# Kernel optimization log

Hardware: AMD Instinct MI355X
Metric: run time of the kernel (lower is better)

## Reference

```python
import jax, jax.numpy as jnp
import numpy as np

B, T, D, L = 8, 8192, 256, 3
DISTS = (1, 5, 15, 30)


def _layernorm(x, g, b, eps=1e-5):
    m = x.mean(-1, keepdims=True)
    v = ((x - m) ** 2).mean(-1, keepdims=True)
    return (x - m) * jax.lax.rsqrt(v + eps) * g + b


def _temporal_edges():
    src, dst = [], []
    for d in DISTS:
        a = np.arange(T - d)
        src += [a, a + d]
        dst += [a + d, a]
    ei = np.stack([np.concatenate(src), np.concatenate(dst)])  # [2, E]
    off = (np.arange(B) * T).repeat(ei.shape[1])
    return np.tile(ei, (1, B)) + off[None, :]  # [2, B*E]


def setup_inputs() -> dict:
    key = jax.random.key(0)
    ks = jax.random.split(key, 6)
    s = 1.0 / np.sqrt(D)
    s4 = 1.0 / np.sqrt(4 * D)
    return dict(
        x=jax.random.normal(ks[0], (B, T, D), jnp.float32),
        adjacency=jnp.zeros((T, T), jnp.float32),  # shape-check only
        edge_index=jnp.asarray(_temporal_edges(), jnp.int32),
        conv_w=jax.random.normal(ks[1], (L, D, D), jnp.float32) * s,
        conv_b=jnp.zeros((L, D), jnp.float32),
        norm_g=jnp.ones((L, D), jnp.float32),
        norm_b=jnp.zeros((L, D), jnp.float32),
        normff_g=jnp.ones((D,), jnp.float32),
        normff_b=jnp.zeros((D,), jnp.float32),
        w1=jax.random.normal(ks[2], (D, 4 * D), jnp.float32) * s,
        b1=jnp.zeros((4 * D,), jnp.float32),
        w2=jax.random.normal(ks[3], (4 * D, D), jnp.float32) * s4,
        b2=jnp.zeros((D,), jnp.float32),
    )


def reference(x, adjacency, edge_index, conv_w, conv_b, norm_g, norm_b,
              normff_g, normff_b, w1, b1, w2, b2):
    b, t, d = x.shape
    n = b * t
    xf = x.reshape(n, d)
    src, dst = edge_index[0], edge_index[1]
    # GCN symmetric degree normalization (no self loops), degrees by target node
    deg = jax.ops.segment_sum(jnp.ones(src.shape[0], x.dtype), dst, num_segments=n)
    dinv = jnp.where(deg > 0, jax.lax.rsqrt(deg), 0.0)
    enorm = (dinv[src] * dinv[dst])[:, None]  # [E,1]
    for i in range(conv_w.shape[0]):
        h = xf @ conv_w[i]                                    # [N,D]
        h = jax.ops.segment_sum(h[src] * enorm, dst, num_segments=n) + conv_b[i]
        h = jax.nn.gelu(h, approximate=False)
        h = _layernorm(h.reshape(b, t, d), norm_g[i], norm_b[i]).reshape(n, d)
        xf = xf + h
    x = xf.reshape(b, t, d)
    y = _layernorm(x, normff_g, normff_b)
    ff = jax.nn.gelu(y @ w1 + b1, approximate=False) @ w2 + b2
    return x + ff
```

## Files before the change

### kernel.cpp

```cpp
#include <hip/hip_runtime.h>
#include <hip/hip_bf16.h>
#include <math.h>
#include <stdint.h>
#include <stddef.h>

#define TB 8
#define TT 8192
#define DD 256
#define NR (TB * TT)
#define HH 1024
#define LL 3

typedef unsigned short ushort_t;
typedef __attribute__((ext_vector_type(8))) short short8;
typedef __attribute__((ext_vector_type(4))) float floatx4;

__device__ __forceinline__ float bf2f(ushort_t u) {
  union { unsigned int i; float f; } x; x.i = ((unsigned int)u) << 16; return x.f;
}
__device__ __forceinline__ ushort_t f2bf(float f) {
  union { float f; unsigned int i; } x; x.f = f;
  unsigned int r = x.i + 0x7fffu + ((x.i >> 16) & 1u);
  return (ushort_t)(r >> 16);
}
__device__ __forceinline__ float ld_in(const void* p, size_t i, int isf) {
  return isf ? ((const float*)p)[i] : bf2f(((const ushort_t*)p)[i]);
}
__device__ __forceinline__ float gelu_f(float v) {
  const float y = v * (0.7978845608028654f + 0.035677408136300125f * v * v);
  const float e = __expf(-2.0f * y);
  return v * __builtin_amdgcn_rcpf(1.0f + e);
}
__device__ __forceinline__ int deg_of(int t) {
  return (t >= 1) + (t >= 5) + (t >= 15) + (t >= 30)
       + (t < TT - 1) + (t < TT - 5) + (t < TT - 15) + (t < TT - 30);
}

__device__ __forceinline__ void gl_lds16(const ushort_t* g, ushort_t* l) {
  __builtin_amdgcn_global_load_lds(
      (const __attribute__((address_space(1))) unsigned int*)(g),
      (__attribute__((address_space(3))) unsigned int*)(l), 16, 0, 0);
}

__device__ __forceinline__ int xcd_swz(int lin, int nwg) {
  const int q = nwg >> 3;
  return (lin & 7) * q + (lin >> 3);
}

__global__ void k_probe(const void* __restrict__ x, int* __restrict__ flag) {
  if (threadIdx.x == 0 && blockIdx.x == 0) {
    const float* fb = (const float*)x;
    int okf = 0;
    for (int i = 0; i < 128; ++i) {
      const float av = fabsf(fb[i]);
      if (av > 1e-6f && av < 100.f) okf++;
    }
    *flag = (okf >= 115) ? 1 : 0;
  }
}

__global__ __launch_bounds__(256) void k_cvt(const void* __restrict__ x,
                                             ushort_t* __restrict__ xb,
                                             const int* __restrict__ flag) {
  const int isf = *flag;
  const size_t i4 = (size_t)blockIdx.x * 256 + threadIdx.x;
  if (isf) {
    const float4 f = ((const float4*)x)[i4];
    ushort4 u; u.x = f2bf(f.x); u.y = f2bf(f.y); u.z = f2bf(f.z); u.w = f2bf(f.w);
    ((ushort4*)xb)[i4] = u;
  } else {
    ((ushort4*)xb)[i4] = ((const ushort4*)x)[i4];
  }
}

__global__ void k_transpose_all(const void* __restrict__ cw,
                                const void* __restrict__ w1,
                                const void* __restrict__ w2,
                                ushort_t* __restrict__ cwT,
                                ushort_t* __restrict__ w1T,
                                ushort_t* __restrict__ w2T,
                                const int* __restrict__ flag) {
  __shared__ ushort_t tile[32][33];
  const int isf = *flag;
  const int b = blockIdx.x;
  const void* src; ushort_t* dst; int R, C, bx, by; size_t row0;
  if (b < 192) {
    const int i = b >> 6, t = b & 63;
    src = cw; dst = cwT + (size_t)i * DD * DD; row0 = (size_t)i * DD;
    R = DD; C = DD; bx = (t & 7) * 32; by = (t >> 3) * 32;
  } else if (b < 448) {
    const int t = b - 192;
    src = w1; dst = w1T; row0 = 0; R = DD; C = HH;
    bx = (t & 31) * 32; by = (t >> 5) * 32;
  } else {
    const int t = b - 448;
    src = w2; dst = w2T; row0 = 0; R = HH; C = DD;
    bx = (t & 7) * 32; by = (t >> 3) * 32;
  }
  const int tx = threadIdx.x;
  for (int i = threadIdx.y; i < 32; i += 8)
    tile[i][tx] = f2bf(ld_in(src, (row0 + by + i) * (size_t)C + bx + tx, isf));
  __syncthreads();
  for (int i = threadIdx.y; i < 32; i += 8)
    dst[(size_t)(bx + i) * R + by + tx] = tile[tx][i];
}

__global__ __launch_bounds__(256, 2) void k_conv_fused(
    const ushort_t* __restrict__ xin, ushort_t* __restrict__ xout,
    const ushort_t* __restrict__ Bt, const void* __restrict__ bias,
    size_t boff, const void* __restrict__ g, const void* __restrict__ bn,
    size_t goff, const int* __restrict__ flag) {
  __shared__ alignas(16) ushort_t smem[35072];
  float* scr      = (float*)smem;
  float* part     = scr;
  float* partsq   = scr + 256;
  float* smu      = scr + 512;
  float* srs      = scr + 576;
  ushort_t* aggA  = smem + 2304;
  ushort_t* Bs    = smem + 18688;
  ushort_t* rt    = smem + 2304;
  const int isf = *flag;

  const int tid  = threadIdx.x;
  const int lane = tid & 63;
  const int l16  = lane & 15;
  const int quad = lane >> 4;
  const int w    = tid >> 6;
  const int m0   = xcd_swz(blockIdx.x, gridDim.x) * 64;

  const int rowt = tid >> 3;
  const int segt = tid & 7;
  const ushort_t* pb = Bt + (size_t)rowt * DD + segt * 8;
  ushort_t* lB = Bs + w * 512;
#pragma unroll
  for (int i = 0; i < 8; ++i)
    gl_lds16(pb + (size_t)i * 32 * DD, lB + i * 2048);

  const int tbase = m0 & (TT - 1);
  const bool interior = (tbase >= 60) && (tbase <= TT - 124);
  const int koffs[8] = {-30, -15, -5, -1, 1, 5, 15, 30};
#pragma unroll
  for (int j = 0; j < 8; ++j) {
    const int id = j * 256 + tid;
    const int r = id >> 5, c = id & 31;
    const ushort_t* base = xin + (size_t)(m0 + r) * DD + c * 8;
    float s[8] = {0.f, 0.f, 0.f, 0.f, 0.f, 0.f, 0.f, 0.f};
    if (interior) {
#pragma unroll
      for (int e = 0; e < 8; ++e) {
        const short8 u = *(const short8*)(base + (ptrdiff_t)koffs[e] * DD);
#pragma unroll
        for (int q2 = 0; q2 < 8; ++q2) s[q2] += bf2f((ushort_t)u[q2]);
      }
#pragma unroll
      for (int q2 = 0; q2 < 8; ++q2) s[q2] *= 0.125f;
    } else {
      const int t = tbase + r;
      const float di = rsqrtf((float)deg_of(t));
#pragma unroll
      for (int e = 0; e < 8; ++e) {
        const int t2 = t + koffs[e];
        if ((unsigned)t2 < (unsigned)TT) {
          const float wgt = di * rsqrtf((float)deg_of(t2));
          const short8 u = *(const short8*)(base + (ptrdiff_t)koffs[e] * DD);
#pragma unroll
          for (int q2 = 0; q2 < 8; ++q2) s[q2] += wgt * bf2f((ushort_t)u[q2]);
        }
      }
    }
    short8 o;
#pragma unroll
    for (int q2 = 0; q2 < 8; ++q2) o[q2] = (short)f2bf(s[q2]);
    *(short8*)(aggA + (c >> 3) * 4096 + r * 64 + (c & 7) * 8) = o;
  }
  __syncthreads();

  floatx4 acc[4][4];
#pragma unroll
  for (int i = 0; i < 4; ++i)
#pragma unroll
    for (int j = 0; j < 4; ++j) acc[i][j] = {0.f, 0.f, 0.f, 0.f};

#pragma unroll
  for (int t = 0; t < 4; ++t) {
    if (t > 0) {
      __syncthreads();
#pragma unroll
      for (int i = 0; i < 8; ++i)
        gl_lds16(pb + t * 64 + (size_t)i * 32 * DD, lB + i * 2048);
      __syncthreads();
    }
    const ushort_t* Ac = aggA + t * 4096;
#pragma unroll
    for (int ks = 0; ks < 2; ++ks) {
      short8 af[4], bfr[4];
#pragma unroll
      for (int mt = 0; mt < 4; ++mt)
        af[mt] = *(const short8*)(Ac + (mt * 16 + l16) * 64 + ks * 32 + quad * 8);
#pragma unroll
      for (int nt = 0; nt < 4; ++nt)
        bfr[nt] = *(const short8*)(Bs + (w * 64 + nt * 16 + l16) * 64 + ks * 32 + quad * 8);
#pragma unroll
      for (int mt = 0; mt < 4; ++mt)
#pragma unroll
        for (int nt = 0; nt < 4; ++nt)
          acc[mt][nt] = __builtin_amdgcn_mfma_f32_16x16x32_bf16(
              af[mt], bfr[nt], acc[mt][nt], 0, 0, 0);
    }
  }

#pragma unroll
  for (int nt = 0; nt < 4; ++nt) {
    const float bv = ld_in(bias, boff + w * 64 + nt * 16 + l16, isf);
#pragma unroll
    for (int mt = 0; mt < 4; ++mt)
#pragma unroll
      for (int r = 0; r < 4; ++r)
        acc[mt][nt][r] = gelu_f(acc[mt][nt][r] + bv);
  }
#pragma unroll
  for (int mt = 0; mt < 4; ++mt) {
#pragma unroll
    for (int r = 0; r < 4; ++r) {
      float p = 0.f, q = 0.f;
#pragma unroll
      for (int nt = 0; nt < 4; ++nt) {
        const float v = acc[mt][nt][r];
        p += v; q += v * v;
      }
#pragma unroll
      for (int o = 8; o > 0; o >>= 1) {
        p += __shfl_xor(p, o, 64);
        q += __shfl_xor(q, o, 64);
      }
      if (l16 == 0) {
        const int rowloc = mt * 16 + quad * 4 + r;
        part[w * 64 + rowloc] = p;
        partsq[w * 64 + rowloc] = q;
      }
    }
  }
  __syncthreads();
  if (tid < 64) {
    const float s  = part[tid] + part[64 + tid] + part[128 + tid] + part[192 + tid];
    const float sq = partsq[tid] + partsq[64 + tid] + partsq[128 + tid] + partsq[192 + tid];
    const float mu = s * (1.0f / DD);
    const float var = sq * (1.0f / DD) - mu * mu;
    smu[tid] = mu;
    srs[tid] = rsqrtf(var + 1e-5f);
  }
  __syncthreads();

#pragma unroll
  for (int nt = 0; nt < 4; ++nt) {
    const int col = w * 64 + nt * 16 + l16;
    const float gv = ld_in(g, goff + col, isf);
    const float bnv = ld_in(bn, goff + col, isf);
#pragma unroll
    for (int mt = 0; mt < 4; ++mt) {
#pragma unroll
      for (int r = 0; r < 4; ++r) {
        const int rowloc = mt * 16 + quad * 4 + r;
        rt[rowloc * 264 + col] =
            f2bf((acc[mt][nt][r] - smu[rowloc]) * srs[rowloc] * gv + bnv);
      }
    }
  }
  __syncthreads();

#pragma unroll
  for (int i = 0; i < 8; ++i) {
    const int ch = tid + i * 256;
    const int row = ch >> 5, sg = ch & 31;
    const short8 xv = *(const short8*)(xin + (size_t)(m0 + row) * DD + sg * 8);
    const short8 rv = *(const short8*)(rt + row * 264 + sg * 8);
    short8 ov;
#pragma unroll
    for (int j = 0; j < 8; ++j)
      ov[j] = (short)f2bf(bf2f((ushort_t)xv[j]) + bf2f((ushort_t)rv[j]));
    *(short8*)(xout + (size_t)(m0 + row) * DD + sg * 8) = ov;
  }
}

__global__ __launch_bounds__(512, 2) void k_ffn(
    const ushort_t* __restrict__ xb, const ushort_t* __restrict__ w1T,
    const ushort_t* __restrict__ w2T, const void* __restrict__ gff,
    const void* __restrict__ bff, const void* __restrict__ b1,
    const void* __restrict__ b2, void* __restrict__ dout,
    const int* __restrict__ flag) {
  __shared__ alignas(16) ushort_t smem[65536];
  ushort_t* An = smem;
  ushort_t* Zs = smem + 32768;
  ushort_t* Bs = smem + 49152;
  ushort_t* Rs = smem + 32768;
  const int isf = *flag;

  const int tid  = threadIdx.x;
  const int lane = tid & 63;
  const int l16  = lane & 15;
  const int quad = lane >> 4;
  const int W    = tid >> 6;
  const int wr   = W >> 2;
  const int wc   = W & 3;
  const int m0   = xcd_swz(blockIdx.x, gridDim.x) * 128;

  const int sg = tid & 31;
  float gffv[8], bffv[8];
#pragma unroll
  for (int j = 0; j < 8; ++j) {
    gffv[j] = ld_in(gff, sg * 8 + j, isf);
    bffv[j] = ld_in(bff, sg * 8 + j, isf);
  }
#pragma unroll
  for (int i = 0; i < 8; ++i) {
    const int row = (tid + i * 512) >> 5;
    const short8 xv = *(const short8*)(xb + (size_t)(m0 + row) * DD + sg * 8);
    float v[8], ps = 0.f, pq = 0.f;
#pragma unroll
    for (int j = 0; j < 8; ++j) {
      v[j] = bf2f((ushort_t)xv[j]); ps += v[j]; pq += v[j] * v[j];
    }
#pragma unroll
    for (int o = 16; o > 0; o >>= 1) {
      ps += __shfl_xor(ps, o, 64);
      pq += __shfl_xor(pq, o, 64);
    }
    const float mu = ps * (1.0f / DD);
    const float rs = rsqrtf(pq * (1.0f / DD) - mu * mu + 1e-5f);
    short8 o8;
#pragma unroll
    for (int j = 0; j < 8; ++j)
      o8[j] = (short)f2bf((v[j] - mu) * rs * gffv[j] + bffv[j]);
    *(short8*)(An + (sg >> 3) * 8192 + row * 64 + (sg & 7) * 8) = o8;
  }

  floatx4 acc2[4][4];
#pragma unroll
  for (int i = 0; i < 4; ++i)
#pragma unroll
    for (int j = 0; j < 4; ++j) acc2[i][j] = {0.f, 0.f, 0.f, 0.f};

  const int rowt = tid >> 3;
  const int segt = tid & 7;
  ushort_t* lB = Bs + W * 512;

  __syncthreads();

  for (int n1 = 0; n1 < 8; ++n1) {
    floatx4 acc1[4][2];
#pragma unroll
    for (int i = 0; i < 4; ++i)
#pragma unroll
      for (int j = 0; j < 2; ++j) acc1[i][j] = {0.f, 0.f, 0.f, 0.f};

#pragma unroll
    for (int kc = 0; kc < 4; ++kc) {
      __syncthreads();
#pragma unroll
      for (int i = 0; i < 2; ++i)
        gl_lds16(w1T + (size_t)(n1 * 128 + i * 64 + rowt) * DD + kc * 64 + segt * 8,
                 lB + i * 4096);
      __syncthreads();
#pragma unroll
      for (int ks = 0; ks < 2; ++ks) {
        short8 af[4], bfr[2];
#pragma unroll
        for (int mt = 0; mt < 4; ++mt)
          af[mt] = *(const short8*)(An + kc * 8192 +
                      (wr * 64 + mt * 16 + l16) * 64 + ks * 32 + quad * 8);
#pragma unroll
        for (int nt = 0; nt < 2; ++nt)
          bfr[nt] = *(const short8*)(Bs +
                      (wc * 32 + nt * 16 + l16) * 64 + ks * 32 + quad * 8);
#pragma unroll
        for (int mt = 0; mt < 4; ++mt)
#pragma unroll
          for (int nt = 0; nt < 2; ++nt)
            acc1[mt][nt] = __builtin_amdgcn_mfma_f32_16x16x32_bf16(
                af[mt], bfr[nt], acc1[mt][nt], 0, 0, 0);
      }
    }

#pragma unroll
    for (int nt = 0; nt < 2; ++nt) {
      const int col = wc * 32 + nt * 16 + l16;
      const float b1v = ld_in(b1, n1 * 128 + col, isf);
#pragma unroll
      for (int mt = 0; mt < 4; ++mt)
#pragma unroll
        for (int r = 0; r < 4; ++r) {
          const int row = wr * 64 + mt * 16 + quad * 4 + r;
          Zs[(col >> 6) * 8192 + row * 64 + (col & 63)] =
              f2bf(gelu_f(acc1[mt][nt][r] + b1v));
        }
    }

#pragma unroll
    for (int kc2 = 0; kc2 < 2; ++kc2) {
      __syncthreads();
#pragma unroll
      for (int i = 0; i < 4; ++i)
        gl_lds16(w2T + (size_t)(i * 64 + rowt) * HH + n1 * 128 + kc2 * 64 + segt * 8,
                 lB + i * 4096);
      __syncthreads();
#pragma unroll
      for (int ks = 0; ks < 2; ++ks) {
        short8 af[4], bfr[4];
#pragma unroll
        for (int mt = 0; mt < 4; ++mt)
          af[mt] = *(const short8*)(Zs + kc2 * 8192 +
                      (wr * 64 + mt * 16 + l16) * 64 + ks * 32 + quad * 8);
#pragma unroll
        for (int nt = 0; nt < 4; ++nt)
          bfr[nt] = *(const short8*)(Bs +
                      (wc * 64 + nt * 16 + l16) * 64 + ks * 32 + quad * 8);
#pragma unroll
        for (int mt = 0; mt < 4; ++mt)
#pragma unroll
          for (int nt = 0; nt < 4; ++nt)
            acc2[mt][nt] = __builtin_amdgcn_mfma_f32_16x16x32_bf16(
                af[mt], bfr[nt], acc2[mt][nt], 0, 0, 0);
      }
    }
  }

  __syncthreads();
#pragma unroll
  for (int i = 0; i < 8; ++i)
    gl_lds16(xb + (size_t)(m0 + i * 16 + (tid >> 5)) * DD + (tid & 31) * 8,
             Rs + i * 4096 + W * 512);
  __syncthreads();

#pragma unroll
  for (int nt = 0; nt < 4; ++nt) {
    const int col = wc * 64 + nt * 16 + l16;
    const float b2v = ld_in(b2, col, isf);
#pragma unroll
    for (int mt = 0; mt < 4; ++mt) {
#pragma unroll
      for (int r = 0; r < 4; ++r) {
        const int lr = wr * 64 + mt * 16 + quad * 4 + r;
        const float v = acc2[mt][nt][r] + b2v + bf2f(Rs[lr * 256 + col]);
        const size_t idx = (size_t)(m0 + lr) * DD + col;
        if (isf) ((float*)dout)[idx] = v;
        else     ((ushort_t*)dout)[idx] = f2bf(v);
      }
    }
  }
}

extern "C" void kernel_launch(void* const* d_in, const int* in_sizes, int n_in,
                              void* d_out, int out_size, void* d_ws, size_t ws_size,
                              hipStream_t stream) {
  const void* x      = d_in[0];
  const void* conv_w = d_in[3];
  const void* conv_b = d_in[4];
  const void* norm_g = d_in[5];
  const void* norm_b = d_in[6];
  const void* nff_g  = d_in[7];
  const void* nff_b  = d_in[8];
  const void* w1     = d_in[9];
  const void* b1     = d_in[10];
  const void* w2     = d_in[11];
  const void* b2     = d_in[12];
  (void)in_sizes; (void)n_in; (void)out_size; (void)ws_size;

  char* ws = (char*)d_ws;
  int*      flag = (int*)ws;      ws += 16;
  ushort_t* xA   = (ushort_t*)ws; ws += (size_t)NR * DD * 2;
  ushort_t* xB   = (ushort_t*)ws; ws += (size_t)NR * DD * 2;
  ushort_t* cwT  = (ushort_t*)ws; ws += (size_t)LL * DD * DD * 2;
  ushort_t* w1T  = (ushort_t*)ws; ws += (size_t)DD * HH * 2;
  ushort_t* w2T  = (ushort_t*)ws; ws += (size_t)HH * DD * 2;

  k_probe<<<1, 64, 0, stream>>>(x, flag);
  k_transpose_all<<<704, dim3(32, 8), 0, stream>>>(
      conv_w, w1, w2, cwT, w1T, w2T, flag);
  k_cvt<<<(NR * DD / 4) / 256, 256, 0, stream>>>(x, xA, flag);

  k_conv_fused<<<NR / 64, 256, 0, stream>>>(
      xA, xB, cwT, conv_b, 0, norm_g, norm_b, 0, flag);
  k_conv_fused<<<NR / 64, 256, 0, stream>>>(
      xB, xA, cwT + (size_t)DD * DD, conv_b, DD, norm_g, norm_b, DD, flag);
  k_conv_fused<<<NR / 64, 256, 0, stream>>>(
      xA, xB, cwT + (size_t)2 * DD * DD, conv_b, 2 * DD, norm_g, norm_b,
      2 * DD, flag);

  k_ffn<<<NR / 128, 512, 0, stream>>>(
      xB, w1T, w2T, nff_g, nff_b, b1, b2, d_out, flag);
}
```

Baseline: 712.4 us.

## Swizzle LDS tiles, per-wave B staging with prefetch, shrink FFN blocks

Adds XOR-swizzled LDS layouts for the A and B tiles to avoid bank conflicts. Each wave now stages its own B slice, and the next k-chunk is prefetched right after the current fragments are read, which replaces the block-wide __syncthreads pairs with waitcnt and s_barrier. The FFN kernel moves from 128-row blocks of 512 threads to 64-row blocks of 256 threads. The conv kernel's LDS footprint roughly doubles, which may reduce occupancy. Correctness now depends on manual waitcnt ordering.

```diff
diff --git a/kernel.cpp b/kernel.cpp
--- a/kernel.cpp
+++ b/kernel.cpp
@@ -35,17 +35,23 @@
   return (t >= 1) + (t >= 5) + (t >= 15) + (t >= 30)
        + (t < TT - 1) + (t < TT - 5) + (t < TT - 15) + (t < TT - 30);
 }
-
-__device__ __forceinline__ void gl_lds16(const ushort_t* g, ushort_t* l) {
+__device__ __forceinline__ void gl_lds16(const ushort_t* g, void* l) {
   __builtin_amdgcn_global_load_lds(
       (const __attribute__((address_space(1))) unsigned int*)(g),
       (__attribute__((address_space(3))) unsigned int*)(l), 16, 0, 0);
 }
-
 __device__ __forceinline__ int xcd_swz(int lin, int nwg) {
   const int q = nwg >> 3;
   return (lin & 7) * q + (lin >> 3);
 }
+__device__ __forceinline__ int swz128(int row, int bytecol) {
+  return row * 128 + (bytecol ^ ((row & 7) << 4));
+}
+__device__ __forceinline__ int swz64(int row, int bytecol) {
+  return row * 64 + (bytecol ^ ((row & 3) << 4));
+}
+#define WAIT_VM0()  asm volatile("s_waitcnt vmcnt(0)" ::: "memory")
+#define WAIT_LGKM0() asm volatile("s_waitcnt lgkmcnt(0)" ::: "memory")
 
 __global__ void k_probe(const void* __restrict__ x, int* __restrict__ flag) {
   if (threadIdx.x == 0 && blockIdx.x == 0) {
@@ -110,15 +116,14 @@
     const ushort_t* __restrict__ Bt, const void* __restrict__ bias,
     size_t boff, const void* __restrict__ g, const void* __restrict__ bn,
     size_t goff, const int* __restrict__ flag) {
-  __shared__ alignas(16) ushort_t smem[35072];
-  float* scr      = (float*)smem;
-  float* part     = scr;
-  float* partsq   = scr + 256;
-  float* smu      = scr + 512;
-  float* srs      = scr + 576;
-  ushort_t* aggA  = smem + 2304;
-  ushort_t* Bs    = smem + 18688;
-  ushort_t* rt    = smem + 2304;
+  __shared__ alignas(16) char smem[68096];
+  float* scr    = (float*)smem;
+  float* part   = scr;
+  float* partsq = scr + 256;
+  float* smu    = scr + 512;
+  float* srs    = scr + 576;
+  char* aggA    = smem + 2560;
+  char* rt      = smem + 2560;
   const int isf = *flag;
 
   const int tid  = threadIdx.x;
@@ -128,13 +133,17 @@
   const int w    = tid >> 6;
   const int m0   = xcd_swz(blockIdx.x, gridDim.x) * 64;
 
-  const int rowt = tid >> 3;
-  const int segt = tid & 7;
-  const ushort_t* pb = Bt + (size_t)rowt * DD + segt * 8;
-  ushort_t* lB = Bs + w * 512;
-#pragma unroll
-  for (int i = 0; i < 8; ++i)
-    gl_lds16(pb + (size_t)i * 32 * DD, lB + i * 2048);
+  char* lB = smem + 35328 + w * 8192;
+
+  const int srow = lane >> 3;
+  const int sseg = (lane & 7) ^ (srow & 7);
+  auto stageB = [&](int kc) {
+#pragma unroll
+    for (int i = 0; i < 8; ++i)
+      gl_lds16(Bt + (size_t)(w * 64 + i * 8 + srow) * DD + kc * 64 + sseg * 8,
+               lB + i * 1024);
+  };
+  stageB(0);
 
   const int tbase = m0 & (TT - 1);
   const bool interior = (tbase >= 60) && (tbase <= TT - 124);
@@ -171,9 +180,11 @@
     short8 o;
 #pragma unroll
     for (int q2 = 0; q2 < 8; ++q2) o[q2] = (short)f2bf(s[q2]);
-    *(short8*)(aggA + (c >> 3) * 4096 + r * 64 + (c & 7) * 8) = o;
-  }
-  __syncthreads();
+    *(short8*)(aggA + (c >> 3) * 8192 + swz128(r, (c & 7) * 16)) = o;
+  }
+  WAIT_LGKM0();
+  __builtin_amdgcn_s_barrier();
+  __builtin_amdgcn_sched_barrier(0);
 
   floatx4 acc[4][4];
 #pragma unroll
@@ -182,31 +193,36 @@
     for (int j = 0; j < 4; ++j) acc[i][j] = {0.f, 0.f, 0.f, 0.f};
 
 #pragma unroll
-  for (int t = 0; t < 4; ++t) {
-    if (t > 0) {
-      __syncthreads();
-#pragma unroll
-      for (int i = 0; i < 8; ++i)
-        gl_lds16(pb + t * 64 + (size_t)i * 32 * DD, lB + i * 2048);
-      __syncthreads();
-    }
-    const ushort_t* Ac = aggA + t * 4096;
-#pragma unroll
-    for (int ks = 0; ks < 2; ++ks) {
-      short8 af[4], bfr[4];
-#pragma unroll
-      for (int mt = 0; mt < 4; ++mt)
-        af[mt] = *(const short8*)(Ac + (mt * 16 + l16) * 64 + ks * 32 + quad * 8);
+  for (int kc = 0; kc < 4; ++kc) {
+    WAIT_VM0();
+    short8 af0[4], bf0[4], af1[4], bf1[4];
+#pragma unroll
+    for (int mt = 0; mt < 4; ++mt) {
+      af0[mt] = *(const short8*)(aggA + kc * 8192 +
+                   swz128(mt * 16 + l16, quad * 16));
+      af1[mt] = *(const short8*)(aggA + kc * 8192 +
+                   swz128(mt * 16 + l16, 64 + quad * 16));
+    }
+#pragma unroll
+    for (int nt = 0; nt < 4; ++nt) {
+      bf0[nt] = *(const short8*)(lB + swz128(nt * 16 + l16, quad * 16));
+      bf1[nt] = *(const short8*)(lB + swz128(nt * 16 + l16, 64 + quad * 16));
+    }
+    WAIT_LGKM0();
+    __builtin_amdgcn_sched_barrier(0);
+    if (kc < 3) stageB(kc + 1);
+#pragma unroll
+    for (int mt = 0; mt < 4; ++mt)
 #pragma unroll
       for (int nt = 0; nt < 4; ++nt)
-        bfr[nt] = *(const short8*)(Bs + (w * 64 + nt * 16 + l16) * 64 + ks * 32 + quad * 8);
-#pragma unroll
-      for (int mt = 0; mt < 4; ++mt)
-#pragma unroll
-        for (int nt = 0; nt < 4; ++nt)
-          acc[mt][nt] = __builtin_amdgcn_mfma_f32_16x16x32_bf16(
-              af[mt], bfr[nt], acc[mt][nt], 0, 0, 0);
-    }
+        acc[mt][nt] = __builtin_amdgcn_mfma_f32_16x16x32_bf16(
+            af0[mt], bf0[nt], acc[mt][nt], 0, 0, 0);
+#pragma unroll
+    for (int mt = 0; mt < 4; ++mt)
+#pragma unroll
+      for (int nt = 0; nt < 4; ++nt)
+        acc[mt][nt] = __builtin_amdgcn_mfma_f32_16x16x32_bf16(
+            af1[mt], bf1[nt], acc[mt][nt], 0, 0, 0);
   }
 
 #pragma unroll
@@ -261,7 +277,7 @@
 #pragma unroll
       for (int r = 0; r < 4; ++r) {
         const int rowloc = mt * 16 + quad * 4 + r;
-        rt[rowloc * 264 + col] =
+        *(ushort_t*)(rt + (rowloc * 264 + col) * 2) =
             f2bf((acc[mt][nt][r] - smu[rowloc]) * srs[rowloc] * gv + bnv);
       }
     }
@@ -273,7 +289,7 @@
     const int ch = tid + i * 256;
     const int row = ch >> 5, sg = ch & 31;
     const short8 xv = *(const short8*)(xin + (size_t)(m0 + row) * DD + sg * 8);
-    const short8 rv = *(const short8*)(rt + row * 264 + sg * 8);
+    const short8 rv = *(const short8*)(rt + (row * 264 + sg * 8) * 2);
     short8 ov;
 #pragma unroll
     for (int j = 0; j < 8; ++j)
@@ -282,27 +298,46 @@
   }
 }
 
-__global__ __launch_bounds__(512, 2) void k_ffn(
+__global__ __launch_bounds__(256, 2) void k_ffn(
     const ushort_t* __restrict__ xb, const ushort_t* __restrict__ w1T,
     const ushort_t* __restrict__ w2T, const void* __restrict__ gff,
     const void* __restrict__ bff, const void* __restrict__ b1,
     const void* __restrict__ b2, void* __restrict__ dout,
     const int* __restrict__ flag) {
-  __shared__ alignas(16) ushort_t smem[65536];
-  ushort_t* An = smem;
-  ushort_t* Zs = smem + 32768;
-  ushort_t* Bs = smem + 49152;
-  ushort_t* Rs = smem + 32768;
+  __shared__ alignas(16) char smem[65536];
+  char* An = smem;
+  char* Zs = smem + 32768;
+  char* Rs = smem;
   const int isf = *flag;
 
   const int tid  = threadIdx.x;
   const int lane = tid & 63;
   const int l16  = lane & 15;
   const int quad = lane >> 4;
-  const int W    = tid >> 6;
-  const int wr   = W >> 2;
-  const int wc   = W & 3;
-  const int m0   = xcd_swz(blockIdx.x, gridDim.x) * 128;
+  const int w    = tid >> 6;
+  const int m0   = xcd_swz(blockIdx.x, gridDim.x) * 64;
+  char* Bw = smem + 49152 + w * 4096;
+
+  const int sr8 = lane >> 3;
+  const int ss8 = (lane & 7) ^ (sr8 & 7);
+  auto stageB1 = [&](int n1, int kc) {
+#pragma unroll
+    for (int i = 0; i < 4; ++i)
+      gl_lds16(w1T + (size_t)(n1 * 128 + w * 32 + i * 8 + sr8) * DD +
+                   kc * 64 + ss8 * 8,
+               Bw + i * 1024);
+  };
+  const int sr4 = lane >> 2;
+  const int ss4 = (lane & 3) ^ (sr4 & 3);
+  auto stageB2 = [&](int n1, int kc2, int ks) {
+#pragma unroll
+    for (int i = 0; i < 4; ++i)
+      gl_lds16(w2T + (size_t)(w * 64 + i * 16 + sr4) * HH +
+                   n1 * 128 + kc2 * 64 + ks * 32 + ss4 * 8,
+               Bw + i * 1024);
+  };
+
+  stageB1(0, 0);
 
   const int sg = tid & 31;
   float gffv[8], bffv[8];
@@ -313,7 +348,7 @@
   }
 #pragma unroll
   for (int i = 0; i < 8; ++i) {
-    const int row = (tid + i * 512) >> 5;
+    const int row = (tid + i * 256) >> 5;
     const short8 xv = *(const short8*)(xb + (size_t)(m0 + row) * DD + sg * 8);
     float v[8], ps = 0.f, pq = 0.f;
 #pragma unroll
@@ -331,20 +366,17 @@
 #pragma unroll
     for (int j = 0; j < 8; ++j)
       o8[j] = (short)f2bf((v[j] - mu) * rs * gffv[j] + bffv[j]);
-    *(short8*)(An + (sg >> 3) * 8192 + row * 64 + (sg & 7) * 8) = o8;
-  }
+    *(short8*)(An + (sg >> 3) * 8192 + swz128(row, (sg & 7) * 16)) = o8;
+  }
+  WAIT_LGKM0();
+  __builtin_amdgcn_s_barrier();
+  __builtin_amdgcn_sched_barrier(0);
 
   floatx4 acc2[4][4];
 #pragma unroll
   for (int i = 0; i < 4; ++i)
 #pragma unroll
     for (int j = 0; j < 4; ++j) acc2[i][j] = {0.f, 0.f, 0.f, 0.f};
-
-  const int rowt = tid >> 3;
-  const int segt = tid & 7;
-  ushort_t* lB = Bs + W * 512;
-
-  __syncthreads();
 
   for (int n1 = 0; n1 < 8; ++n1) {
     floatx4 acc1[4][2];
@@ -355,65 +387,74 @@
 
 #pragma unroll
     for (int kc = 0; kc < 4; ++kc) {
-      __syncthreads();
-#pragma unroll
-      for (int i = 0; i < 2; ++i)
-        gl_lds16(w1T + (size_t)(n1 * 128 + i * 64 + rowt) * DD + kc * 64 + segt * 8,
-                 lB + i * 4096);
-      __syncthreads();
-#pragma unroll
-      for (int ks = 0; ks < 2; ++ks) {
-        short8 af[4], bfr[2];
-#pragma unroll
-        for (int mt = 0; mt < 4; ++mt)
-          af[mt] = *(const short8*)(An + kc * 8192 +
-                      (wr * 64 + mt * 16 + l16) * 64 + ks * 32 + quad * 8);
+      WAIT_VM0();
+      short8 af0[4], af1[4], bq0[2], bq1[2];
+#pragma unroll
+      for (int mt = 0; mt < 4; ++mt)
+        af0[mt] = *(const short8*)(An + kc * 8192 +
+                     swz128(mt * 16 + l16, quad * 16));
+#pragma unroll
+      for (int nt = 0; nt < 2; ++nt)
+        bq0[nt] = *(const short8*)(Bw + swz128(nt * 16 + l16, quad * 16));
+#pragma unroll
+      for (int mt = 0; mt < 4; ++mt)
 #pragma unroll
         for (int nt = 0; nt < 2; ++nt)
-          bfr[nt] = *(const short8*)(Bs +
-                      (wc * 32 + nt * 16 + l16) * 64 + ks * 32 + quad * 8);
-#pragma unroll
-        for (int mt = 0; mt < 4; ++mt)
-#pragma unroll
-          for (int nt = 0; nt < 2; ++nt)
-            acc1[mt][nt] = __builtin_amdgcn_mfma_f32_16x16x32_bf16(
-                af[mt], bfr[nt], acc1[mt][nt], 0, 0, 0);
-      }
+          acc1[mt][nt] = __builtin_amdgcn_mfma_f32_16x16x32_bf16(
+              af0[mt], bq0[nt], acc1[mt][nt], 0, 0, 0);
+#pragma unroll
+      for (int mt = 0; mt < 4; ++mt)
+        af1[mt] = *(const short8*)(An + kc * 8192 +
+                     swz128(mt * 16 + l16, 64 + quad * 16));
+#pragma unroll
+      for (int nt = 0; nt < 2; ++nt)
+        bq1[nt] = *(const short8*)(Bw + swz128(nt * 16 + l16, 64 + quad * 16));
+      WAIT_LGKM0();
+      __builtin_amdgcn_sched_barrier(0);
+      if (kc < 3) stageB1(n1, kc + 1);
+#pragma unroll
+      for (int mt = 0; mt < 4; ++mt)
+#pragma unroll
+        for (int nt = 0; nt < 2; ++nt)
+          acc1[mt][nt] = __builtin_amdgcn_mfma_f32_16x16x32_bf16(
+              af1[mt], bq1[nt], acc1[mt][nt], 0, 0, 0);
     }
 
 #pragma unroll
     for (int nt = 0; nt < 2; ++nt) {
-      const int col = wc * 32 + nt * 16 + l16;
+      const int col = w * 32 + nt * 16 + l16;
       const float b1v = ld_in(b1, n1 * 128 + col, isf);
 #pragma unroll
       for (int mt = 0; mt < 4; ++mt)
 #pragma unroll
         for (int r = 0; r < 4; ++r) {
-          const int row = wr * 64 + mt * 16 + quad * 4 + r;
-          Zs[(col >> 6) * 8192 + row * 64 + (col & 63)] =
+          const int row = mt * 16 + quad * 4 + r;
+          *(ushort_t*)(Zs + (col >> 6) * 8192 + swz128(row, (col & 63) * 2)) =
               f2bf(gelu_f(acc1[mt][nt][r] + b1v));
         }
     }
+    stageB2(n1, 0, 0);
+    WAIT_LGKM0();
+    __builtin_amdgcn_s_barrier();
+    __builtin_amdgcn_sched_barrier(0);
 
 #pragma unroll
     for (int kc2 = 0; kc2 < 2; ++kc2) {
-      __syncthreads();
-#pragma unroll
-      for (int i = 0; i < 4; ++i)
-        gl_lds16(w2T + (size_t)(i * 64 + rowt) * HH + n1 * 128 + kc2 * 64 + segt * 8,
-                 lB + i * 4096);
-      __syncthreads();
 #pragma unroll
       for (int ks = 0; ks < 2; ++ks) {
+        WAIT_VM0();
         short8 af[4], bfr[4];
 #pragma unroll
         for (int mt = 0; mt < 4; ++mt)
           af[mt] = *(const short8*)(Zs + kc2 * 8192 +
-                      (wr * 64 + mt * 16 + l16) * 64 + ks * 32 + quad * 8);
+                     swz128(mt * 16 + l16, ks * 64 + quad * 16));
 #pragma unroll
         for (int nt = 0; nt < 4; ++nt)
-          bfr[nt] = *(const short8*)(Bs +
-                      (wc * 64 + nt * 16 + l16) * 64 + ks * 32 + quad * 8);
+          bfr[nt] = *(const short8*)(Bw + swz64(nt * 16 + l16, quad * 16));
+        WAIT_LGKM0();
+        __builtin_amdgcn_sched_barrier(0);
+        if (kc2 == 0 || ks == 0) stageB2(n1, kc2 + (ks & 1), (ks + 1) & 1);
+        else if (n1 < 7) stageB1(n1 + 1, 0);
 #pragma unroll
         for (int mt = 0; mt < 4; ++mt)
 #pragma unroll
@@ -422,25 +463,29 @@
                 af[mt], bfr[nt], acc2[mt][nt], 0, 0, 0);
       }
     }
-  }
-
+    __builtin_amdgcn_s_barrier();
+    __builtin_amdgcn_sched_barrier(0);
+  }
+
+  WAIT_VM0();
+#pragma unroll
+  for (int i = 0; i < 8; ++i)
+    gl_lds16(xb + (size_t)(m0 + ((i * 256 + tid) >> 5)) * DD +
+                 ((i * 256 + tid) & 31) * 8,
+             Rs + i * 4096 + w * 1024);
   __syncthreads();
-#pragma unroll
-  for (int i = 0; i < 8; ++i)
-    gl_lds16(xb + (size_t)(m0 + i * 16 + (tid >> 5)) * DD + (tid & 31) * 8,
-             Rs + i * 4096 + W * 512);
-  __syncthreads();
 
 #pragma unroll
   for (int nt = 0; nt < 4; ++nt) {
-    const int col = wc * 64 + nt * 16 + l16;
+    const int col = w * 64 + nt * 16 + l16;
     const float b2v = ld_in(b2, col, isf);
 #pragma unroll
     for (int mt = 0; mt < 4; ++mt) {
 #pragma unroll
       for (int r = 0; r < 4; ++r) {
-        const int lr = wr * 64 + mt * 16 + quad * 4 + r;
-        const float v = acc2[mt][nt][r] + b2v + bf2f(Rs[lr * 256 + col]);
+        const int lr = mt * 16 + quad * 4 + r;
+        const float v = acc2[mt][nt][r] + b2v +
+                        bf2f(*(const ushort_t*)(Rs + lr * 512 + col * 2));
         const size_t idx = (size_t)(m0 + lr) * DD + col;
         if (isf) ((float*)dout)[idx] = v;
         else     ((ushort_t*)dout)[idx] = f2bf(v);
@@ -486,6 +531,6 @@
       xA, xB, cwT + (size_t)2 * DD * DD, conv_b, 2 * DD, norm_g, norm_b,
       2 * DD, flag);
 
-  k_ffn<<<NR / 128, 512, 0, stream>>>(
+  k_ffn<<<NR / 64, 256, 0, stream>>>(
       xB, w1T, w2T, nff_g, nff_b, b1, b2, d_out, flag);
 }
```

After: 640.6 us. 1.11x faster.
